# Performance work log

Hardware: AMD Instinct MI355X
Metric: run time of the kernel (lower is better)

The kernel has to match this reference:

```python
import jax, jax.numpy as jnp
import numpy as np

V, D, T, B, MS, WIN, EOS = 10000, 256, 128, 8, 4, 1, 4
S = MS + 1          # decoder segment length (y_input0 + MAX_SEGMENT tokens)
HRATE = 0.1
LOGINF = 1e6


def setup_inputs() -> dict:
    key = jax.random.key(0)
    ks = jax.random.split(key, 17)
    s = lambda i, shape: (jax.random.normal(ks[i], shape, jnp.float32) * 0.05)
    return dict(
        x_ids=jax.random.randint(ks[0], (B, T + 2 * WIN), 0, V),
        lens=jnp.full((B,), T, dtype=jnp.int32),
        emb=s(1, (V, D)),
        y_start=s(2, (1, D)),
        cell_Wi=s(3, (4 * D, D)), cell_Wh=s(4, (4 * D, D)), cell_b=s(5, (4 * D,)),
        yin0_W=s(6, (D, D)), yin0_b=s(7, (D,)),
        hlin_W=s(8, (2 * D, D)), hlin_b=s(9, (2 * D,)),
        l0_Wi=s(10, (4 * D, D)), l0_Wh=s(11, (4 * D, D)), l0_b=s(12, (4 * D,)),
        l1_Wi=s(13, (4 * D, D)), l1_Wh=s(14, (4 * D, D)), l1_b=s(15, (4 * D,)),
        out_b=s(16, (V,)),
    )


def _cell(x, h, c, Wi, Wh, b):
    # torch LSTM gate order: i, f, g, o
    g = x @ Wi.T + h @ Wh.T + b
    i, f, gg, o = jnp.split(g, 4, axis=-1)
    c2 = jax.nn.sigmoid(f) * c + jax.nn.sigmoid(i) * jnp.tanh(gg)
    return jax.nn.sigmoid(o) * jnp.tanh(c2), c2


def reference(x_ids, lens, emb, y_start, cell_Wi, cell_Wh, cell_b,
              yin0_W, yin0_b, hlin_W, hlin_b,
              l0_Wi, l0_Wh, l0_b, l1_Wi, l1_Wh, l1_b, out_b):
    y = x_ids[:, WIN:-WIN]                     # [B, T] target ids
    x = emb[y]                                 # [B, T, D]

    # --- encoder LSTMCell scan over j_start (state persists across schedule) ---
    seq = jnp.concatenate(
        [jnp.broadcast_to(y_start, (B, D))[None], jnp.transpose(x, (1, 0, 2))[:-1]], 0)  # [T,B,D]
    z = jnp.zeros((B, D), x.dtype)
    def enc_step(carry, xt):
        h, c = carry
        h2, c2 = _cell(xt, h, c, cell_Wi, cell_Wh, cell_b)
        return (h2, c2), h2
    _, h_seq = jax.lax.scan(enc_step, (z, z), seq)        # [T, B, D]

    drop_h = HRATE * h_seq
    y_in0 = drop_h @ yin0_W.T + yin0_b                    # [T, B, D]
    h0_all = jnp.tanh(drop_h @ hlin_W.T + hlin_b).reshape(T, B, 2, D)  # per-layer init h

    # --- build decoder inputs [T, B, S, D]: (y_input0, x[j_start:j_start+MS]) ---
    xp = jnp.pad(x, ((0, 0), (0, MS), (0, 0)))            # zero-pad time (causal => pads don't affect valid outputs)
    pos = jnp.arange(T)[:, None] + jnp.arange(MS)[None, :]           # [T, MS]
    seg_x = jnp.transpose(xp[:, pos], (1, 0, 2, 3))       # [T, B, MS, D]
    seg = jnp.concatenate([y_in0[:, :, None, :], seg_x], axis=2)     # [T, B, S, D]

    # --- 2-layer LSTM decoder, vmapped over j_start ---
    def decode(seg_t, h_init):                            # seg_t [B,S,D], h_init [B,2,D]
        def step(carry, xt):
            (h0, c0), (h1, c1) = carry
            h0n, c0n = _cell(xt, h0, c0, l0_Wi, l0_Wh, l0_b)
            h1n, c1n = _cell(h0n, h1, c1, l1_Wi, l1_Wh, l1_b)
            return ((h0n, c0n), (h1n, c1n)), h1n
        init = ((h_init[:, 0], z), (h_init[:, 1], z))
        _, hs = jax.lax.scan(step, init, jnp.transpose(seg_t, (1, 0, 2)))
        return jnp.transpose(hs, (1, 0, 2))               # [B, S, D]
    dec_h = jax.vmap(decode)(seg, h0_all)                 # [T, B, S, D]

    # --- tied output projection + log-softmax (only needed gathers kept) ---
    logits = jnp.einsum('tbsd,vd->tbsv', dec_h, emb) + out_b         # [T,B,S,V]
    logZ = jax.nn.logsumexp(logits, axis=-1)                          # [T,B,S]

    tgt = jnp.transpose(y[:, jnp.clip(pos, 0, T - 1)], (1, 0, 2))     # [T,B,MS]
    tgt_lp = jnp.take_along_axis(logits[:, :, :MS, :], tgt[..., None], axis=3)[..., 0] \
             - logZ[:, :, :MS]                                        # [T,B,MS]
    pmask = (pos < T)[:, None, :]
    cum = jnp.cumsum(jnp.where(pmask, tgt_lp, 0.0), axis=2)           # [T,B,MS]
    eos_lp = logits[:, :, 1:, EOS] - logZ[:, :, 1:]                   # [T,B,MS]

    kmask = (jnp.arange(T)[:, None] + jnp.arange(1, MS + 1)[None, :]) <= T   # [T,MS]
    body = jnp.where(kmask[:, None, :], cum + eos_lp, -LOGINF)        # [T,B,MS]
    logpy = jnp.concatenate([jnp.full((T, 1, B), -LOGINF, body.dtype),
                             jnp.transpose(body, (0, 2, 1))], axis=1)  # [T, MS+1, B]

    # --- alpha forward DP: alpha[j] = logsumexp_L alpha[j-L] + logpy[j-L][L] ---
    jj = jnp.arange(1, T + 1)[:, None]
    ii = jnp.arange(MS)[None, :]
    sstart = jj - MS + ii                                             # [T,MS]
    LPG = jnp.where((sstart >= 0)[..., None],
                    logpy[jnp.clip(sstart, 0), jnp.broadcast_to(MS - ii, (T, MS))],
                    -LOGINF)                                          # [T,MS,B]

    Apad0 = jnp.full((MS + T + 1, B), -LOGINF, logpy.dtype).at[MS].set(0.0)
    def dp_step(Apad, args):
        j, lpg = args
        win = jax.lax.dynamic_slice(Apad, (j, 0), (MS, B))            # alpha[j-MS .. j-1]
        aj = jax.nn.logsumexp(win + lpg, axis=0)
        return jax.lax.dynamic_update_slice(Apad, aj[None], (MS + j, 0)), None
    Apad, _ = jax.lax.scan(dp_step, Apad0, (jnp.arange(1, T + 1), LPG))
    alpha = Apad[MS:]                                                 # [T+1, B]

    ret = -jnp.sum(alpha[lens, jnp.arange(B)]) / jnp.sum(lens).astype(alpha.dtype)
    return ret
```

## Files before the change

### kernel.cpp

```cpp
#include <hip/hip_runtime.h>

#define V_ 10000
#define D_ 256
#define T_ 128
#define B_ 8
#define MS_ 4
#define S_ 5
#define EOS_ 4

typedef unsigned short b16_t;
typedef __attribute__((ext_vector_type(8))) short s16x8;
typedef __attribute__((ext_vector_type(8))) unsigned short u16x8;
typedef __attribute__((ext_vector_type(4))) float f32x4;
typedef __attribute__((ext_vector_type(2))) _Float16 h16x2;

__device__ inline b16_t f2bf(float f) {
  union { float f; unsigned u; } v; v.f = f;
  unsigned r = v.u + 0x7FFFu + ((v.u >> 16) & 1u);
  return (b16_t)(r >> 16);
}
__device__ inline float bf2f(b16_t h) {
  union { unsigned u; float f; } v; v.u = ((unsigned)h) << 16; return v.f;
}
__device__ inline float sigm_(float x) { return 1.0f / (1.0f + __expf(-x)); }
__device__ inline float tanh_(float x) { return 2.0f / (1.0f + __expf(-2.0f * x)) - 1.0f; }
__device__ inline h16x2 bch(unsigned u) { return __builtin_bit_cast(h16x2, u); }
__device__ inline unsigned pkh(float a, float b) {
  h16x2 v; v.x = (_Float16)a; v.y = (_Float16)b;
  return __builtin_bit_cast(unsigned, v);
}

#if __has_builtin(__builtin_amdgcn_fdot2)
#define FDOT2(a, b, c) __builtin_amdgcn_fdot2((a), (b), (c), false)
#else
#define FDOT2(a, b, c) ((c) + (float)(a).x * (float)(b).x + (float)(a).y * (float)(b).y)
#endif

__device__ inline void cvt4(const float* __restrict__ s, b16_t* __restrict__ d) {
  float4 v = *(const float4*)s;
  ushort4 o = { f2bf(v.x), f2bf(v.y), f2bf(v.z), f2bf(v.w) };
  *(ushort4*)d = o;
}

__global__ void k_prep(const float* __restrict__ emb, const float* __restrict__ cWi,
                       const float* __restrict__ y0W, const float* __restrict__ hlW,
                       const float* __restrict__ l0Wi, const float* __restrict__ l0Wh,
                       const float* __restrict__ l1Wi, const float* __restrict__ l1Wh,
                       const float* __restrict__ cWh, const int* __restrict__ x_ids,
                       const float* __restrict__ y_st,
                       b16_t* __restrict__ emb_bf, b16_t* __restrict__ cWi_bf,
                       b16_t* __restrict__ y0W_bf, b16_t* __restrict__ hlW_bf,
                       b16_t* __restrict__ l0Wi_bf, b16_t* __restrict__ l0Wh_bf,
                       b16_t* __restrict__ Wcat_bf, unsigned* __restrict__ Whf,
                       b16_t* __restrict__ x_bf, b16_t* __restrict__ seq_bf) {
  for (long i = (long)blockIdx.x * blockDim.x + threadIdx.x; i < 1213440L;
       i += (long)gridDim.x * blockDim.x) {
    if (i < 640000L) { cvt4(emb + i * 4, emb_bf + i * 4); }
    else if (i < 705536L) { long j = i - 640000L; cvt4(cWi + j * 4, cWi_bf + j * 4); }
    else if (i < 721920L) { long j = i - 705536L; cvt4(y0W + j * 4, y0W_bf + j * 4); }
    else if (i < 754688L) { long j = i - 721920L; cvt4(hlW + j * 4, hlW_bf + j * 4); }
    else if (i < 820224L) { long j = i - 754688L; cvt4(l0Wi + j * 4, l0Wi_bf + j * 4); }
    else if (i < 885760L) { long j = i - 820224L; cvt4(l0Wh + j * 4, l0Wh_bf + j * 4); }
    else if (i < 1016832L) {
      long j = (i - 885760L) * 4;
      long n = j >> 9; int k = (int)(j & 511);
      const float* src = (k < 256) ? (l1Wi + n * 256 + k) : (l1Wh + n * 256 + (k - 256));
      cvt4(src, Wcat_bf + j);
    } else if (i < 1082368L) {
      long j = i - 1016832L;
      float4 v = *(const float4*)(cWh + j * 4);
      Whf[2 * j] = pkh(v.x, v.y);
      Whf[2 * j + 1] = pkh(v.z, v.w);
    } else if (i < 1147904L) {
      long j = i - 1082368L;
      int bt = (int)(j >> 6), c = (int)(j & 63) * 4;
      int b = bt >> 7, t = bt & 127;
      int tok = x_ids[b * (T_ + 2) + t + 1];
      cvt4(emb + (size_t)tok * D_ + c, x_bf + (size_t)bt * D_ + c);
    } else {
      long j = i - 1147904L;
      int m = (int)(j >> 6), c = (int)(j & 63) * 4;
      int t = m >> 3, b = m & 7;
      const float* src = (t == 0) ? (y_st + c)
                                  : (emb + (size_t)x_ids[b * (T_ + 2) + t] * D_ + c);
      cvt4(src, seq_bf + (size_t)m * D_ + c);
    }
  }
}

__global__ __launch_bounds__(256) void k_gemm(const b16_t* __restrict__ A,
                                              const b16_t* __restrict__ Bw,
                                              const float* __restrict__ bias,
                                              float* __restrict__ C,
                                              int N, int act, int obf) {
  __shared__ b16_t As[64][264];
  __shared__ b16_t Bs[64][264];
  int tid = threadIdx.x;
  int rowBase = blockIdx.x * 64, colBase = blockIdx.y * 64;
  for (int i = tid; i < 64 * 32; i += 256) {
    int r = i >> 5, c = (i & 31) * 8;
    *(u16x8*)&As[r][c] = *(const u16x8*)(A + (size_t)(rowBase + r) * D_ + c);
    *(u16x8*)&Bs[r][c] = *(const u16x8*)(Bw + (size_t)(colBase + r) * D_ + c);
  }
  __syncthreads();
  int w = tid >> 6, l = tid & 63, lr = l & 15, kg = l >> 4;
  f32x4 acc[4] = {{0.f,0.f,0.f,0.f},{0.f,0.f,0.f,0.f},{0.f,0.f,0.f,0.f},{0.f,0.f,0.f,0.f}};
  for (int kk = 0; kk < 8; ++kk) {
    s16x8 a = *(const s16x8*)&As[w * 16 + lr][kk * 32 + kg * 8];
#pragma unroll
    for (int f = 0; f < 4; ++f) {
      s16x8 b = *(const s16x8*)&Bs[f * 16 + lr][kk * 32 + kg * 8];
      acc[f] = __builtin_amdgcn_mfma_f32_16x16x32_bf16(a, b, acc[f], 0, 0, 0);
    }
  }
#pragma unroll
  for (int f = 0; f < 4; ++f) {
#pragma unroll
    for (int r = 0; r < 4; ++r) {
      int m = rowBase + w * 16 + kg * 4 + r;
      int n = colBase + f * 16 + lr;
      float v = acc[f][r];
      if (bias) v += bias[n];
      if (act == 1) v = tanh_(v);
      size_t idx = (size_t)m * N + n;
      if (obf) ((b16_t*)C)[idx] = f2bf(v); else C[idx] = v;
    }
  }
}

__global__ __launch_bounds__(512, 2) void k_encoder(
    const unsigned* __restrict__ Whf,
    const float* __restrict__ encX,
    unsigned* __restrict__ hglob,
    int* __restrict__ flags,
    b16_t* __restrict__ droph) {
  int batch = blockIdx.x & 7, half = blockIdx.x >> 3;
  int tid = threadIdx.x;
  int gate = tid & 3, dl = tid >> 2;
  int dim = half * 128 + dl;
  int row = gate * 256 + dim;
  unsigned wv[128];
  {
    const uint4* wp = (const uint4*)(Whf + (size_t)row * 128);
#pragma unroll
    for (int i = 0; i < 32; ++i) {
      uint4 v = wp[i];
      wv[4 * i + 0] = v.x; wv[4 * i + 1] = v.y;
      wv[4 * i + 2] = v.z; wv[4 * i + 3] = v.w;
    }
  }
#pragma unroll
  for (int i = 0; i < 128; ++i) asm volatile("" : "+v"(wv[i]));

  __shared__ unsigned hbuf[2][128];
  if (tid < 256) ((unsigned*)hbuf)[tid] = 0;
  __syncthreads();

  float c = 0.f;
  int p = 0;
#pragma unroll 1
  for (int t = 0; t < 128; ++t) {
    float a = encX[((size_t)t * 8 + batch) * 1024 + row];
    uint4 hv[8];
#pragma unroll
    for (int i = 0; i < 8; ++i) hv[i] = *(const uint4*)&hbuf[p][i * 4];
    float s0 = 0.f, s1 = 0.f, s2 = 0.f, s3 = 0.f;
#pragma unroll
    for (int i = 0; i < 8; ++i) {
      s0 = FDOT2(bch(hv[i].x), bch(wv[4 * i + 0]), s0);
      s1 = FDOT2(bch(hv[i].y), bch(wv[4 * i + 1]), s1);
      s2 = FDOT2(bch(hv[i].z), bch(wv[4 * i + 2]), s2);
      s3 = FDOT2(bch(hv[i].w), bch(wv[4 * i + 3]), s3);
    }
    float acc = a + (s0 + s1) + (s2 + s3);
    int base = (tid & 63) & ~3;
    float gi = __shfl(acc, base + 0, 64);
    float gf = __shfl(acc, base + 1, 64);
    float gg = __shfl(acc, base + 2, 64);
    float go = __shfl(acc, base + 3, 64);
    float c2 = sigm_(gf) * c + sigm_(gi) * tanh_(gg);
    float h2 = sigm_(go) * tanh_(c2);
    c = c2;
    int q = p ^ 1;
    if (gate == 0) {
      ((_Float16*)hbuf[q])[dim] = (_Float16)h2;
      droph[((size_t)t * 8 + batch) * 256 + dim] = f2bf(0.1f * h2);
    }
    __syncthreads();
    if (t < 127) {
      if (tid < 64) {
        unsigned dw = hbuf[q][half * 64 + tid];
        __hip_atomic_store(&hglob[((size_t)(t + 1) * 8 + batch) * 128 + half * 64 + tid],
                           dw, __ATOMIC_RELAXED, __HIP_MEMORY_SCOPE_AGENT);
        asm volatile("s_waitcnt vmcnt(0)" ::: "memory");
        if (tid == 0)
          __hip_atomic_store(&flags[((t + 1) * 8 + batch) * 2 + half], 1,
                             __ATOMIC_RELAXED, __HIP_MEMORY_SCOPE_AGENT);
      } else if (tid < 128) {
        int lane = tid - 64;
        int* fp = &flags[((t + 1) * 8 + batch) * 2 + (1 - half)];
        while (__hip_atomic_load(fp, __ATOMIC_RELAXED, __HIP_MEMORY_SCOPE_AGENT) == 0)
          __builtin_amdgcn_s_sleep(1);
        asm volatile("" ::: "memory");
        unsigned dw = __hip_atomic_load(
            &hglob[((size_t)(t + 1) * 8 + batch) * 128 + (1 - half) * 64 + lane],
            __ATOMIC_RELAXED, __HIP_MEMORY_SCOPE_AGENT);
        hbuf[q][(1 - half) * 64 + lane] = dw;
      }
    }
    __syncthreads();
    p = q;
  }
}

__global__ void k_seg(const b16_t* __restrict__ x_bf, const b16_t* __restrict__ y_in0_bf,
                      b16_t* __restrict__ seg_bf) {
  int ps = blockIdx.x, d = threadIdx.x;
  int p = ps / S_, s = ps % S_;
  int t = p >> 3, b = p & 7;
  b16_t v;
  if (s == 0) v = y_in0_bf[(size_t)p * D_ + d];
  else {
    int tt = t + s - 1;
    v = (tt < T_) ? x_bf[((size_t)b * T_ + tt) * D_ + d] : (b16_t)0;
  }
  seg_bf[(size_t)ps * D_ + d] = v;
}

template <int K, int PHASE>
__global__ __launch_bounds__(512, 2) void k_dec_step(
    b16_t* __restrict__ hcat,
    const b16_t* __restrict__ Wbf,
    const float* __restrict__ X0,
    const float* __restrict__ bias,
    float* __restrict__ cst,
    b16_t* __restrict__ dec_out,
    int s) {
  __shared__ b16_t As[16][(K == 256) ? 264 : 520];
  __shared__ float gacc[16][1028];
  int tid = threadIdx.x;
  int R0 = blockIdx.x * 16;
  constexpr int CH = K / 8;
  for (int i = tid; i < 16 * CH; i += 512) {
    int r = i / CH, cc = (i % CH) * 8;
    *(u16x8*)&As[r][cc] = *(const u16x8*)(hcat + (size_t)(R0 + r) * 512 + cc);
  }
  __syncthreads();
  int w = tid >> 6, l = tid & 63, lr = l & 15, kg = l >> 4;
  int g = w >> 1, ch = w & 1;
  constexpr int NK = K / 32;
  s16x8 af[NK];
#pragma unroll
  for (int kk = 0; kk < NK; ++kk) af[kk] = *(const s16x8*)&As[lr][kk * 32 + kg * 8];
  int ncol0 = g * 256 + ch * 128;
  f32x4 acc[8];
#pragma unroll
  for (int nt = 0; nt < 8; ++nt) acc[nt] = f32x4{0.f, 0.f, 0.f, 0.f};
#pragma unroll
  for (int nt = 0; nt < 8; ++nt) {
    int n = ncol0 + nt * 16 + lr;
    const b16_t* bp = Wbf + (size_t)n * K + kg * 8;
#pragma unroll
    for (int kk = 0; kk < NK; ++kk) {
      s16x8 bf = *(const s16x8*)(bp + kk * 32);
      acc[nt] = __builtin_amdgcn_mfma_f32_16x16x32_bf16(af[kk], bf, acc[nt], 0, 0, 0);
    }
  }
#pragma unroll
  for (int nt = 0; nt < 8; ++nt)
#pragma unroll
    for (int r = 0; r < 4; ++r)
      gacc[kg * 4 + r][ncol0 + nt * 16 + lr] = acc[nt][r];
  __syncthreads();
  int rr = tid >> 5, dq = tid & 31;
  int pidx = R0 + rr;
#pragma unroll
  for (int u = 0; u < 8; ++u) {
    int d = u * 32 + dq;
    float gi = gacc[rr][d], gf = gacc[rr][256 + d];
    float gg = gacc[rr][512 + d], go = gacc[rr][768 + d];
    if (PHASE == 0) {
      const float* xp = X0 + ((size_t)pidx * 5 + s) * 1024;
      gi += xp[d]; gf += xp[256 + d]; gg += xp[512 + d]; go += xp[768 + d];
    } else {
      gi += bias[d]; gf += bias[256 + d]; gg += bias[512 + d]; go += bias[768 + d];
    }
    float c = cst[(size_t)pidx * 256 + d];
    float c2 = sigm_(gf) * c + sigm_(gi) * tanh_(gg);
    float h2 = sigm_(go) * tanh_(c2);
    cst[(size_t)pidx * 256 + d] = c2;
    b16_t hb = f2bf(h2);
    if (PHASE == 0) hcat[(size_t)pidx * 512 + d] = hb;
    else {
      hcat[(size_t)pidx * 512 + 256 + d] = hb;
      dec_out[((size_t)pidx * 5 + s) * 256 + d] = hb;
    }
  }
}

__global__ __launch_bounds__(512) void k_logits(const b16_t* __restrict__ Abf,
                                                const b16_t* __restrict__ emb_bf,
                                                const float* __restrict__ out_b,
                                                float* __restrict__ sumexp) {
  __shared__ b16_t Bs[64][264];
  int tid = threadIdx.x;
  int rowBase = blockIdx.x * 128;
  int w = tid >> 6, l = tid & 63, lr = l & 15, kg = l >> 4;
  s16x8 af[8];
  {
    const b16_t* arow = Abf + (size_t)(rowBase + w * 16 + lr) * 256;
#pragma unroll
    for (int kk = 0; kk < 8; ++kk) af[kk] = *(const s16x8*)(arow + kk * 32 + kg * 8);
  }
  float runsum[4] = {0.f, 0.f, 0.f, 0.f};
  int t0 = blockIdx.y * 23, t1 = (t0 + 23 < 157) ? (t0 + 23) : 157;
  for (int tile = t0; tile < t1; ++tile) {
    int colBase = tile * 64;
    __syncthreads();
    for (int i = tid; i < 64 * 32; i += 512) {
      int r = i >> 5, cc = (i & 31) * 8;
      int vrow = colBase + r;
      u16x8 bv = {0, 0, 0, 0, 0, 0, 0, 0};
      if (vrow < V_) bv = *(const u16x8*)(emb_bf + (size_t)vrow * D_ + cc);
      *(u16x8*)&Bs[r][cc] = bv;
    }
    __syncthreads();
    f32x4 acc[4] = {{0.f,0.f,0.f,0.f},{0.f,0.f,0.f,0.f},{0.f,0.f,0.f,0.f},{0.f,0.f,0.f,0.f}};
#pragma unroll
    for (int kk = 0; kk < 8; ++kk) {
#pragma unroll
      for (int f = 0; f < 4; ++f) {
        s16x8 b = *(const s16x8*)&Bs[f * 16 + lr][kk * 32 + kg * 8];
        acc[f] = __builtin_amdgcn_mfma_f32_16x16x32_bf16(af[kk], b, acc[f], 0, 0, 0);
      }
    }
#pragma unroll
    for (int f = 0; f < 4; ++f) {
      int n = colBase + f * 16 + lr;
      if (n < V_) {
        float ob = out_b[n];
#pragma unroll
        for (int r = 0; r < 4; ++r) runsum[r] += __expf(acc[f][r] + ob);
      }
    }
  }
#pragma unroll
  for (int r = 0; r < 4; ++r) {
    float rs = runsum[r];
    rs += __shfl_xor(rs, 1, 64);
    rs += __shfl_xor(rs, 2, 64);
    rs += __shfl_xor(rs, 4, 64);
    rs += __shfl_xor(rs, 8, 64);
    if (lr == 0) atomicAdd(&sumexp[rowBase + w * 16 + kg * 4 + r], rs);
  }
}

__global__ void k_extract(const b16_t* __restrict__ dec_h, const b16_t* __restrict__ emb_bf,
                          const float* __restrict__ out_b, const int* __restrict__ x_ids,
                          float* __restrict__ tl, float* __restrict__ el) {
  int p = blockIdx.x, lane = threadIdx.x;
  int t = p >> 3, b = p & 7;
  for (int s = 0; s < S_; ++s) {
    const b16_t* hr = dec_h + ((size_t)p * S_ + s) * D_;
    float hv[4];
#pragma unroll
    for (int j = 0; j < 4; ++j) hv[j] = bf2f(hr[lane * 4 + j]);
    if (s < MS_) {
      int pos = t + s; if (pos > T_ - 1) pos = T_ - 1;
      int tok = x_ids[b * (T_ + 2) + pos + 1];
      const b16_t* er = emb_bf + (size_t)tok * D_;
      float ps = 0.f;
#pragma unroll
      for (int j = 0; j < 4; ++j) ps += hv[j] * bf2f(er[lane * 4 + j]);
      for (int m = 1; m < 64; m <<= 1) ps += __shfl_xor(ps, m, 64);
      if (lane == 0) tl[p * MS_ + s] = ps + out_b[tok];
    }
    if (s >= 1) {
      const b16_t* er = emb_bf + (size_t)EOS_ * D_;
      float ps = 0.f;
#pragma unroll
      for (int j = 0; j < 4; ++j) ps += hv[j] * bf2f(er[lane * 4 + j]);
      for (int m = 1; m < 64; m <<= 1) ps += __shfl_xor(ps, m, 64);
      if (lane == 0) el[p * MS_ + (s - 1)] = ps + out_b[EOS_];
    }
  }
}

__global__ __launch_bounds__(256) void k_final(const float* __restrict__ sumexp,
                                               const float* __restrict__ tl,
                                               const float* __restrict__ el,
                                               const int* __restrict__ lens,
                                               float* __restrict__ out) {
  __shared__ float logpy[T_][S_][B_];
  __shared__ float alpha[T_ + 1][B_];
  int tid = threadIdx.x;
  for (int p = tid; p < T_ * B_; p += 256) {
    int t = p >> 3, b = p & 7;
    float lz[S_];
#pragma unroll
    for (int s = 0; s < S_; ++s) lz[s] = __logf(sumexp[p * S_ + s]);
    float cum = 0.f, cums[MS_];
#pragma unroll
    for (int s = 0; s < MS_; ++s) {
      float tlp = tl[p * MS_ + s] - lz[s];
      if (t + s < T_) cum += tlp;
      cums[s] = cum;
    }
#pragma unroll
    for (int k = 1; k <= MS_; ++k) {
      float bv = -1000000.0f;
      if (t + k <= T_) bv = cums[k - 1] + (el[p * MS_ + (k - 1)] - lz[k]);
      logpy[t][k][b] = bv;
    }
  }
  __syncthreads();
  if (tid < B_) {
    int b = tid;
    alpha[0][b] = 0.f;
    for (int j = 1; j <= T_; ++j) {
      float vs[MS_], vmax = -1e30f;
#pragma unroll
      for (int k = 1; k <= MS_; ++k) {
        float vv = -2000000.0f;
        if (j - k >= 0) vv = alpha[j - k][b] + logpy[j - k][k][b];
        vs[k - 1] = vv;
        if (vv > vmax) vmax = vv;
      }
      float ssum = 0.f;
#pragma unroll
      for (int k = 0; k < MS_; ++k) ssum += __expf(vs[k] - vmax);
      alpha[j][b] = vmax + __logf(ssum);
    }
  }
  __syncthreads();
  if (tid == 0) {
    float num = 0.f, den = 0.f;
    for (int b = 0; b < B_; ++b) { num += alpha[lens[b]][b]; den += (float)lens[b]; }
    out[0] = -num / den;
  }
}

extern "C" void kernel_launch(void* const* d_in, const int* in_sizes, int n_in,
                              void* d_out, int out_size, void* d_ws, size_t ws_size,
                              hipStream_t stream) {
  const int* x_ids   = (const int*)d_in[0];
  const int* lens    = (const int*)d_in[1];
  const float* emb   = (const float*)d_in[2];
  const float* y_st  = (const float*)d_in[3];
  const float* cWi   = (const float*)d_in[4];
  const float* cWh   = (const float*)d_in[5];
  const float* cb    = (const float*)d_in[6];
  const float* y0W   = (const float*)d_in[7];
  const float* y0b   = (const float*)d_in[8];
  const float* hlW   = (const float*)d_in[9];
  const float* hlb   = (const float*)d_in[10];
  const float* l0Wi  = (const float*)d_in[11];
  const float* l0Wh  = (const float*)d_in[12];
  const float* l0b   = (const float*)d_in[13];
  const float* l1Wi  = (const float*)d_in[14];
  const float* l1Wh  = (const float*)d_in[15];
  const float* l1b   = (const float*)d_in[16];
  const float* outb  = (const float*)d_in[17];
  float* out = (float*)d_out;
  (void)in_sizes; (void)n_in; (void)out_size; (void)ws_size;

  char* ws = (char*)d_ws;
  size_t cur = 0;
  auto alloc = [&](size_t bytes) { size_t o = cur; cur += (bytes + 255) & ~(size_t)255; return o; };
  b16_t* emb_bf    = (b16_t*)(ws + alloc((size_t)V_ * D_ * 2));
  b16_t* cWi_bf    = (b16_t*)(ws + alloc(1024 * 256 * 2));
  b16_t* y0W_bf    = (b16_t*)(ws + alloc(256 * 256 * 2));
  b16_t* hlW_bf    = (b16_t*)(ws + alloc(512 * 256 * 2));
  b16_t* l0Wi_bf   = (b16_t*)(ws + alloc(1024 * 256 * 2));
  b16_t* l0Wh_bf   = (b16_t*)(ws + alloc(1024 * 256 * 2));
  b16_t* Wcat_bf   = (b16_t*)(ws + alloc(1024 * 512 * 2));
  unsigned* Whf    = (unsigned*)(ws + alloc(1024 * 128 * 4));
  b16_t* x_bf      = (b16_t*)(ws + alloc((size_t)B_ * T_ * D_ * 2));
  b16_t* seq_bf    = (b16_t*)(ws + alloc(1024 * 256 * 2));
  float* encX      = (float*)(ws + alloc((size_t)1024 * 1024 * 4));
  b16_t* droph_bf  = (b16_t*)(ws + alloc(1024 * 256 * 2));
  b16_t* y_in0_bf  = (b16_t*)(ws + alloc(1024 * 256 * 2));
  b16_t* hcat      = (b16_t*)(ws + alloc(1024 * 512 * 2));
  b16_t* seg_bf    = (b16_t*)(ws + alloc((size_t)5120 * 256 * 2));
  float* X0        = (float*)(ws + alloc((size_t)5120 * 1024 * 4));
  float* c0        = (float*)(ws + alloc((size_t)2 * 1024 * 256 * 4));
  float* c1        = c0 + 1024 * 256;
  b16_t* dec_h_bf  = (b16_t*)(ws + alloc((size_t)5120 * 256 * 2));
  float* sumexp    = (float*)(ws + alloc(5120 * 4));
  int* flags       = (int*)(ws + alloc(129 * 8 * 2 * 4));
  unsigned* hglob  = (unsigned*)(ws + alloc((size_t)129 * 8 * 128 * 4));
  float* tl        = (float*)(ws + alloc(1024 * MS_ * 4));
  float* el        = (float*)(ws + alloc(1024 * MS_ * 4));

  hipMemsetAsync(sumexp, 0, 20480 + 8256, stream);
  hipMemsetAsync(c0, 0, (size_t)2 * 1024 * 256 * 4, stream);

  k_prep<<<1024, 256, 0, stream>>>(emb, cWi, y0W, hlW, l0Wi, l0Wh, l1Wi, l1Wh, cWh,
                                   x_ids, y_st,
                                   emb_bf, cWi_bf, y0W_bf, hlW_bf, l0Wi_bf, l0Wh_bf,
                                   Wcat_bf, Whf, x_bf, seq_bf);

  k_gemm<<<dim3(16, 16), 256, 0, stream>>>(seq_bf, cWi_bf, cb, encX, 1024, 0, 0);
  k_encoder<<<16, 512, 0, stream>>>(Whf, encX, hglob, flags, droph_bf);

  k_gemm<<<dim3(16, 4), 256, 0, stream>>>(droph_bf, y0W_bf, y0b, (float*)y_in0_bf, 256, 0, 1);
  k_gemm<<<dim3(16, 8), 256, 0, stream>>>(droph_bf, hlW_bf, hlb, (float*)hcat, 512, 1, 1);
  k_seg<<<5120, 256, 0, stream>>>(x_bf, y_in0_bf, seg_bf);
  k_gemm<<<dim3(80, 16), 256, 0, stream>>>(seg_bf, l0Wi_bf, l0b, X0, 1024, 0, 0);

  for (int s = 0; s < S_; ++s) {
    k_dec_step<256, 0><<<64, 512, 0, stream>>>(hcat, l0Wh_bf, X0, nullptr, c0, nullptr, s);
    k_dec_step<512, 1><<<64, 512, 0, stream>>>(hcat, Wcat_bf, nullptr, l1b, c1, dec_h_bf, s);
  }

  k_logits<<<dim3(40, 7), 512, 0, stream>>>(dec_h_bf, emb_bf, outb, sumexp);
  k_extract<<<1024, 64, 0, stream>>>(dec_h_bf, emb_bf, outb, x_ids, tl, el);
  k_final<<<1, 256, 0, stream>>>(sumexp, tl, el, lens, out);
}
```

Before: 676.8 us.

## Single-block encoder per batch, overlap X0 GEMM with encoder, fuse decoder layers

The encoder now uses one 512-thread block per batch row, holding the recurrent weights in registers plus LDS instead of splitting across two blocks that synchronise through global flags. Extra blocks in the same launch compute the token-dependent part of the layer-0 input projection while the serial encoder runs. The y_in0 column of that projection is done later with strided GEMM calls. Segment building moves into the prep kernel, the two decoder layers are fused into one kernel per step, and the logits grid is split finer. This removes inter-block spin-waits and several launches, at the cost of higher register and LDS pressure and fewer blocks in the decoder.

```diff
diff --git a/kernel.cpp b/kernel.cpp
--- a/kernel.cpp
+++ b/kernel.cpp
@@ -52,8 +52,8 @@
                        b16_t* __restrict__ y0W_bf, b16_t* __restrict__ hlW_bf,
                        b16_t* __restrict__ l0Wi_bf, b16_t* __restrict__ l0Wh_bf,
                        b16_t* __restrict__ Wcat_bf, unsigned* __restrict__ Whf,
-                       b16_t* __restrict__ x_bf, b16_t* __restrict__ seq_bf) {
-  for (long i = (long)blockIdx.x * blockDim.x + threadIdx.x; i < 1213440L;
+                       b16_t* __restrict__ seq_bf, b16_t* __restrict__ seg_bf) {
+  for (long i = (long)blockIdx.x * blockDim.x + threadIdx.x; i < 1410048L;
        i += (long)gridDim.x * blockDim.x) {
     if (i < 640000L) { cvt4(emb + i * 4, emb_bf + i * 4); }
     else if (i < 705536L) { long j = i - 640000L; cvt4(cWi + j * 4, cWi_bf + j * 4); }
@@ -73,34 +73,42 @@
       Whf[2 * j + 1] = pkh(v.z, v.w);
     } else if (i < 1147904L) {
       long j = i - 1082368L;
-      int bt = (int)(j >> 6), c = (int)(j & 63) * 4;
-      int b = bt >> 7, t = bt & 127;
-      int tok = x_ids[b * (T_ + 2) + t + 1];
-      cvt4(emb + (size_t)tok * D_ + c, x_bf + (size_t)bt * D_ + c);
-    } else {
-      long j = i - 1147904L;
       int m = (int)(j >> 6), c = (int)(j & 63) * 4;
       int t = m >> 3, b = m & 7;
       const float* src = (t == 0) ? (y_st + c)
                                   : (emb + (size_t)x_ids[b * (T_ + 2) + t] * D_ + c);
       cvt4(src, seq_bf + (size_t)m * D_ + c);
-    }
-  }
-}
-
-__global__ __launch_bounds__(256) void k_gemm(const b16_t* __restrict__ A,
+    } else {
+      long j = i - 1147904L;
+      int r = (int)(j >> 6), c = (int)(j & 63) * 4;
+      int p = r >> 2, s = 1 + (r & 3);
+      int t = p >> 3, b = p & 7;
+      int tt = t + s - 1;
+      int ps = r + (r >> 2) + 1;
+      if (tt < T_) {
+        int tok = x_ids[b * (T_ + 2) + tt + 1];
+        cvt4(emb + (size_t)tok * D_ + c, seg_bf + (size_t)ps * 256 + c);
+      } else {
+        ushort4 z = {0, 0, 0, 0};
+        *(ushort4*)(seg_bf + (size_t)ps * 256 + c) = z;
+      }
+    }
+  }
+}
+
+__global__ __launch_bounds__(256) void k_gemm(const b16_t* __restrict__ A, int lda,
                                               const b16_t* __restrict__ Bw,
                                               const float* __restrict__ bias,
-                                              float* __restrict__ C,
-                                              int N, int act, int obf) {
+                                              float* __restrict__ C, int ldc,
+                                              int act, int obf) {
   __shared__ b16_t As[64][264];
   __shared__ b16_t Bs[64][264];
   int tid = threadIdx.x;
   int rowBase = blockIdx.x * 64, colBase = blockIdx.y * 64;
   for (int i = tid; i < 64 * 32; i += 256) {
     int r = i >> 5, c = (i & 31) * 8;
-    *(u16x8*)&As[r][c] = *(const u16x8*)(A + (size_t)(rowBase + r) * D_ + c);
-    *(u16x8*)&Bs[r][c] = *(const u16x8*)(Bw + (size_t)(colBase + r) * D_ + c);
+    *(u16x8*)&As[r][c] = *(const u16x8*)(A + (size_t)(rowBase + r) * lda + c);
+    *(u16x8*)&Bs[r][c] = *(const u16x8*)(Bw + (size_t)(colBase + r) * 256 + c);
   }
   __syncthreads();
   int w = tid >> 6, l = tid & 63, lr = l & 15, kg = l >> 4;
@@ -122,178 +130,224 @@
       float v = acc[f][r];
       if (bias) v += bias[n];
       if (act == 1) v = tanh_(v);
-      size_t idx = (size_t)m * N + n;
+      size_t idx = (size_t)m * ldc + n;
       if (obf) ((b16_t*)C)[idx] = f2bf(v); else C[idx] = v;
     }
   }
 }
 
-__global__ __launch_bounds__(512, 2) void k_encoder(
-    const unsigned* __restrict__ Whf,
-    const float* __restrict__ encX,
-    unsigned* __restrict__ hglob,
-    int* __restrict__ flags,
-    b16_t* __restrict__ droph) {
-  int batch = blockIdx.x & 7, half = blockIdx.x >> 3;
+struct EncSmem { uint4 wtail4[16][512]; unsigned hbuf[128]; float gl[1024]; };
+struct GemSmem { b16_t As[64][264]; };
+
+__global__ __launch_bounds__(512, 2) void k_enc_x0(
+    const unsigned* __restrict__ Whf, const float* __restrict__ encX,
+    b16_t* __restrict__ droph,
+    const b16_t* __restrict__ seg_bf, const b16_t* __restrict__ l0Wi_bf,
+    const float* __restrict__ l0b, float* __restrict__ X0) {
+  __shared__ union { EncSmem e; GemSmem g; } sm;
   int tid = threadIdx.x;
-  int gate = tid & 3, dl = tid >> 2;
-  int dim = half * 128 + dl;
-  int row = gate * 256 + dim;
-  unsigned wv[128];
-  {
-    const uint4* wp = (const uint4*)(Whf + (size_t)row * 128);
-#pragma unroll
-    for (int i = 0; i < 32; ++i) {
-      uint4 v = wp[i];
-      wv[4 * i + 0] = v.x; wv[4 * i + 1] = v.y;
-      wv[4 * i + 2] = v.z; wv[4 * i + 3] = v.w;
-    }
-  }
-#pragma unroll
-  for (int i = 0; i < 128; ++i) asm volatile("" : "+v"(wv[i]));
-
-  __shared__ unsigned hbuf[2][128];
-  if (tid < 256) ((unsigned*)hbuf)[tid] = 0;
-  __syncthreads();
-
-  float c = 0.f;
-  int p = 0;
+  if (blockIdx.x < 8) {
+    int batch = blockIdx.x;
+    int r0 = tid, r1 = tid + 512;
+    unsigned wa[96], wb[96];
+    {
+      const uint4* p0 = (const uint4*)(Whf + (size_t)r0 * 128);
+      const uint4* p1 = (const uint4*)(Whf + (size_t)r1 * 128);
+#pragma unroll
+      for (int i = 0; i < 24; ++i) {
+        uint4 v = p0[i];
+        wa[4*i] = v.x; wa[4*i+1] = v.y; wa[4*i+2] = v.z; wa[4*i+3] = v.w;
+      }
+#pragma unroll
+      for (int i = 0; i < 24; ++i) {
+        uint4 v = p1[i];
+        wb[4*i] = v.x; wb[4*i+1] = v.y; wb[4*i+2] = v.z; wb[4*i+3] = v.w;
+      }
+#pragma unroll
+      for (int i = 0; i < 8; ++i) sm.e.wtail4[i][tid] = p0[24 + i];
+#pragma unroll
+      for (int i = 0; i < 8; ++i) sm.e.wtail4[8 + i][tid] = p1[24 + i];
+    }
+#pragma unroll
+    for (int i = 0; i < 96; ++i) asm volatile("v_mov_b32 %0, %0" : "+v"(wa[i]));
+#pragma unroll
+    for (int i = 0; i < 96; ++i) asm volatile("v_mov_b32 %0, %0" : "+v"(wb[i]));
+    if (tid < 128) sm.e.hbuf[tid] = 0;
+    float c = 0.f;
+    __syncthreads();
 #pragma unroll 1
-  for (int t = 0; t < 128; ++t) {
-    float a = encX[((size_t)t * 8 + batch) * 1024 + row];
-    uint4 hv[8];
-#pragma unroll
-    for (int i = 0; i < 8; ++i) hv[i] = *(const uint4*)&hbuf[p][i * 4];
-    float s0 = 0.f, s1 = 0.f, s2 = 0.f, s3 = 0.f;
-#pragma unroll
-    for (int i = 0; i < 8; ++i) {
-      s0 = FDOT2(bch(hv[i].x), bch(wv[4 * i + 0]), s0);
-      s1 = FDOT2(bch(hv[i].y), bch(wv[4 * i + 1]), s1);
-      s2 = FDOT2(bch(hv[i].z), bch(wv[4 * i + 2]), s2);
-      s3 = FDOT2(bch(hv[i].w), bch(wv[4 * i + 3]), s3);
-    }
-    float acc = a + (s0 + s1) + (s2 + s3);
-    int base = (tid & 63) & ~3;
-    float gi = __shfl(acc, base + 0, 64);
-    float gf = __shfl(acc, base + 1, 64);
-    float gg = __shfl(acc, base + 2, 64);
-    float go = __shfl(acc, base + 3, 64);
-    float c2 = sigm_(gf) * c + sigm_(gi) * tanh_(gg);
-    float h2 = sigm_(go) * tanh_(c2);
-    c = c2;
-    int q = p ^ 1;
-    if (gate == 0) {
-      ((_Float16*)hbuf[q])[dim] = (_Float16)h2;
-      droph[((size_t)t * 8 + batch) * 256 + dim] = f2bf(0.1f * h2);
+    for (int t = 0; t < 128; ++t) {
+      const float* ex = encX + ((size_t)t * 8 + batch) * 1024;
+      float a0 = ex[r0], a1 = ex[r1];
+      float s0 = 0.f, s1 = 0.f, s2 = 0.f, s3 = 0.f;
+#pragma unroll
+      for (int j = 0; j < 24; ++j) {
+        uint4 hv = *(const uint4*)&sm.e.hbuf[4 * j];
+        s0 = FDOT2(bch(hv.x), bch(wa[4*j+0]), s0);
+        s0 = FDOT2(bch(hv.y), bch(wa[4*j+1]), s0);
+        s1 = FDOT2(bch(hv.z), bch(wa[4*j+2]), s1);
+        s1 = FDOT2(bch(hv.w), bch(wa[4*j+3]), s1);
+        s2 = FDOT2(bch(hv.x), bch(wb[4*j+0]), s2);
+        s2 = FDOT2(bch(hv.y), bch(wb[4*j+1]), s2);
+        s3 = FDOT2(bch(hv.z), bch(wb[4*j+2]), s3);
+        s3 = FDOT2(bch(hv.w), bch(wb[4*j+3]), s3);
+      }
+#pragma unroll
+      for (int j = 0; j < 8; ++j) {
+        uint4 hv = *(const uint4*)&sm.e.hbuf[96 + 4 * j];
+        uint4 w0 = sm.e.wtail4[j][tid];
+        uint4 w1 = sm.e.wtail4[8 + j][tid];
+        s0 = FDOT2(bch(hv.x), bch(w0.x), s0);
+        s0 = FDOT2(bch(hv.y), bch(w0.y), s0);
+        s1 = FDOT2(bch(hv.z), bch(w0.z), s1);
+        s1 = FDOT2(bch(hv.w), bch(w0.w), s1);
+        s2 = FDOT2(bch(hv.x), bch(w1.x), s2);
+        s2 = FDOT2(bch(hv.y), bch(w1.y), s2);
+        s3 = FDOT2(bch(hv.z), bch(w1.z), s3);
+        s3 = FDOT2(bch(hv.w), bch(w1.w), s3);
+      }
+      sm.e.gl[r0] = a0 + s0 + s1;
+      sm.e.gl[r1] = a1 + s2 + s3;
+      __syncthreads();
+      if (tid < 256) {
+        float gi = sm.e.gl[tid],       gf = sm.e.gl[256 + tid];
+        float gg = sm.e.gl[512 + tid], go = sm.e.gl[768 + tid];
+        float c2 = sigm_(gf) * c + sigm_(gi) * tanh_(gg);
+        float h2 = sigm_(go) * tanh_(c2);
+        c = c2;
+        droph[((size_t)t * 8 + batch) * 256 + tid] = f2bf(0.1f * h2);
+        ((_Float16*)sm.e.hbuf)[tid] = (_Float16)h2;
+      }
+      __syncthreads();
+    }
+  } else {
+    int g = blockIdx.x - 8;
+    int j0 = g * 64;
+    for (int i = tid; i < 64 * 32; i += 512) {
+      int r = i >> 5, cc = (i & 31) * 8;
+      int jj = j0 + r, ps = jj + (jj >> 2) + 1;
+      *(u16x8*)&sm.g.As[r][cc] = *(const u16x8*)(seg_bf + (size_t)ps * 256 + cc);
     }
     __syncthreads();
-    if (t < 127) {
-      if (tid < 64) {
-        unsigned dw = hbuf[q][half * 64 + tid];
-        __hip_atomic_store(&hglob[((size_t)(t + 1) * 8 + batch) * 128 + half * 64 + tid],
-                           dw, __ATOMIC_RELAXED, __HIP_MEMORY_SCOPE_AGENT);
-        asm volatile("s_waitcnt vmcnt(0)" ::: "memory");
-        if (tid == 0)
-          __hip_atomic_store(&flags[((t + 1) * 8 + batch) * 2 + half], 1,
-                             __ATOMIC_RELAXED, __HIP_MEMORY_SCOPE_AGENT);
-      } else if (tid < 128) {
-        int lane = tid - 64;
-        int* fp = &flags[((t + 1) * 8 + batch) * 2 + (1 - half)];
-        while (__hip_atomic_load(fp, __ATOMIC_RELAXED, __HIP_MEMORY_SCOPE_AGENT) == 0)
-          __builtin_amdgcn_s_sleep(1);
-        asm volatile("" ::: "memory");
-        unsigned dw = __hip_atomic_load(
-            &hglob[((size_t)(t + 1) * 8 + batch) * 128 + (1 - half) * 64 + lane],
-            __ATOMIC_RELAXED, __HIP_MEMORY_SCOPE_AGENT);
-        hbuf[q][(1 - half) * 64 + lane] = dw;
-      }
-    }
-    __syncthreads();
-    p = q;
-  }
-}
-
-__global__ void k_seg(const b16_t* __restrict__ x_bf, const b16_t* __restrict__ y_in0_bf,
-                      b16_t* __restrict__ seg_bf) {
-  int ps = blockIdx.x, d = threadIdx.x;
-  int p = ps / S_, s = ps % S_;
-  int t = p >> 3, b = p & 7;
-  b16_t v;
-  if (s == 0) v = y_in0_bf[(size_t)p * D_ + d];
-  else {
-    int tt = t + s - 1;
-    v = (tt < T_) ? x_bf[((size_t)b * T_ + tt) * D_ + d] : (b16_t)0;
-  }
-  seg_bf[(size_t)ps * D_ + d] = v;
-}
-
-template <int K, int PHASE>
-__global__ __launch_bounds__(512, 2) void k_dec_step(
+    int w = tid >> 6, l = tid & 63, lr = l & 15, kg = l >> 4;
+    int mt = w & 3, hn = w >> 2;
+    s16x8 af[8];
+#pragma unroll
+    for (int kk = 0; kk < 8; ++kk)
+      af[kk] = *(const s16x8*)&sm.g.As[mt * 16 + lr][kk * 32 + kg * 8];
+#pragma unroll 1
+    for (int nb = 0; nb < 4; ++nb) {
+      int nc0 = hn * 512 + nb * 128;
+      f32x4 acc[8];
+#pragma unroll
+      for (int nt = 0; nt < 8; ++nt) acc[nt] = f32x4{0.f, 0.f, 0.f, 0.f};
+#pragma unroll
+      for (int nt = 0; nt < 8; ++nt) {
+        int n = nc0 + nt * 16 + lr;
+        const b16_t* bp = l0Wi_bf + (size_t)n * 256 + kg * 8;
+#pragma unroll
+        for (int kk = 0; kk < 8; ++kk)
+          acc[nt] = __builtin_amdgcn_mfma_f32_16x16x32_bf16(
+              af[kk], *(const s16x8*)(bp + kk * 32), acc[nt], 0, 0, 0);
+      }
+#pragma unroll
+      for (int nt = 0; nt < 8; ++nt) {
+        int n = nc0 + nt * 16 + lr;
+        float ob = l0b[n];
+#pragma unroll
+        for (int r = 0; r < 4; ++r) {
+          int jj = j0 + mt * 16 + kg * 4 + r;
+          int ps = jj + (jj >> 2) + 1;
+          X0[(size_t)ps * 1024 + n] = acc[nt][r] + ob;
+        }
+      }
+    }
+  }
+}
+
+__global__ __launch_bounds__(512) void k_dec2(
     b16_t* __restrict__ hcat,
-    const b16_t* __restrict__ Wbf,
+    const b16_t* __restrict__ l0Wh_bf,
+    const b16_t* __restrict__ Wcat_bf,
     const float* __restrict__ X0,
-    const float* __restrict__ bias,
-    float* __restrict__ cst,
-    b16_t* __restrict__ dec_out,
-    int s) {
-  __shared__ b16_t As[16][(K == 256) ? 264 : 520];
-  __shared__ float gacc[16][1028];
+    const float* __restrict__ l1b,
+    float* __restrict__ c0, float* __restrict__ c1,
+    b16_t* __restrict__ dec_out, int s) {
+  __shared__ b16_t A0s[32][264];
+  __shared__ b16_t A1s[32][520];
   int tid = threadIdx.x;
-  int R0 = blockIdx.x * 16;
-  constexpr int CH = K / 8;
-  for (int i = tid; i < 16 * CH; i += 512) {
-    int r = i / CH, cc = (i % CH) * 8;
-    *(u16x8*)&As[r][cc] = *(const u16x8*)(hcat + (size_t)(R0 + r) * 512 + cc);
+  int R0 = blockIdx.x * 32;
+  for (int i = tid; i < 32 * 32; i += 512) {
+    int r = i >> 5, cc = (i & 31) * 8;
+    *(u16x8*)&A0s[r][cc] = *(const u16x8*)(hcat + (size_t)(R0 + r) * 512 + cc);
+    *(u16x8*)&A1s[r][256 + cc] = *(const u16x8*)(hcat + (size_t)(R0 + r) * 512 + 256 + cc);
   }
   __syncthreads();
   int w = tid >> 6, l = tid & 63, lr = l & 15, kg = l >> 4;
-  int g = w >> 1, ch = w & 1;
-  constexpr int NK = K / 32;
-  s16x8 af[NK];
-#pragma unroll
-  for (int kk = 0; kk < NK; ++kk) af[kk] = *(const s16x8*)&As[lr][kk * 32 + kg * 8];
-  int ncol0 = g * 256 + ch * 128;
-  f32x4 acc[8];
-#pragma unroll
-  for (int nt = 0; nt < 8; ++nt) acc[nt] = f32x4{0.f, 0.f, 0.f, 0.f};
-#pragma unroll
-  for (int nt = 0; nt < 8; ++nt) {
-    int n = ncol0 + nt * 16 + lr;
-    const b16_t* bp = Wbf + (size_t)n * K + kg * 8;
-#pragma unroll
-    for (int kk = 0; kk < NK; ++kk) {
-      s16x8 bf = *(const s16x8*)(bp + kk * 32);
-      acc[nt] = __builtin_amdgcn_mfma_f32_16x16x32_bf16(af[kk], bf, acc[nt], 0, 0, 0);
-    }
-  }
-#pragma unroll
-  for (int nt = 0; nt < 8; ++nt)
-#pragma unroll
-    for (int r = 0; r < 4; ++r)
-      gacc[kg * 4 + r][ncol0 + nt * 16 + lr] = acc[nt][r];
+  int m2 = w & 1, dg = w >> 1;
+  s16x8 af[8];
+#pragma unroll
+  for (int kk = 0; kk < 8; ++kk)
+    af[kk] = *(const s16x8*)&A0s[m2 * 16 + lr][kk * 32 + kg * 8];
+#pragma unroll 1
+  for (int dt = 0; dt < 4; ++dt) {
+    int d = dg * 64 + dt * 16 + lr;
+    f32x4 ai{}, afv{}, ag{}, ao{};
+#pragma unroll
+    for (int kk = 0; kk < 8; ++kk) {
+      ai  = __builtin_amdgcn_mfma_f32_16x16x32_bf16(af[kk],
+              *(const s16x8*)(l0Wh_bf + (size_t)(d) * 256 + kk * 32 + kg * 8), ai, 0, 0, 0);
+      afv = __builtin_amdgcn_mfma_f32_16x16x32_bf16(af[kk],
+              *(const s16x8*)(l0Wh_bf + (size_t)(256 + d) * 256 + kk * 32 + kg * 8), afv, 0, 0, 0);
+      ag  = __builtin_amdgcn_mfma_f32_16x16x32_bf16(af[kk],
+              *(const s16x8*)(l0Wh_bf + (size_t)(512 + d) * 256 + kk * 32 + kg * 8), ag, 0, 0, 0);
+      ao  = __builtin_amdgcn_mfma_f32_16x16x32_bf16(af[kk],
+              *(const s16x8*)(l0Wh_bf + (size_t)(768 + d) * 256 + kk * 32 + kg * 8), ao, 0, 0, 0);
+    }
+#pragma unroll
+    for (int r = 0; r < 4; ++r) {
+      int p = R0 + m2 * 16 + kg * 4 + r;
+      const float* xp = X0 + ((size_t)p * 5 + s) * 1024;
+      float gi = ai[r] + xp[d],        gf = afv[r] + xp[256 + d];
+      float gg = ag[r] + xp[512 + d],  go = ao[r] + xp[768 + d];
+      float c = c0[(size_t)p * 256 + d];
+      float c2 = sigm_(gf) * c + sigm_(gi) * tanh_(gg);
+      float h2 = sigm_(go) * tanh_(c2);
+      c0[(size_t)p * 256 + d] = c2;
+      b16_t hb = f2bf(h2);
+      A1s[m2 * 16 + kg * 4 + r][d] = hb;
+      hcat[(size_t)p * 512 + d] = hb;
+    }
+  }
   __syncthreads();
-  int rr = tid >> 5, dq = tid & 31;
-  int pidx = R0 + rr;
-#pragma unroll
-  for (int u = 0; u < 8; ++u) {
-    int d = u * 32 + dq;
-    float gi = gacc[rr][d], gf = gacc[rr][256 + d];
-    float gg = gacc[rr][512 + d], go = gacc[rr][768 + d];
-    if (PHASE == 0) {
-      const float* xp = X0 + ((size_t)pidx * 5 + s) * 1024;
-      gi += xp[d]; gf += xp[256 + d]; gg += xp[512 + d]; go += xp[768 + d];
-    } else {
-      gi += bias[d]; gf += bias[256 + d]; gg += bias[512 + d]; go += bias[768 + d];
-    }
-    float c = cst[(size_t)pidx * 256 + d];
-    float c2 = sigm_(gf) * c + sigm_(gi) * tanh_(gg);
-    float h2 = sigm_(go) * tanh_(c2);
-    cst[(size_t)pidx * 256 + d] = c2;
-    b16_t hb = f2bf(h2);
-    if (PHASE == 0) hcat[(size_t)pidx * 512 + d] = hb;
-    else {
-      hcat[(size_t)pidx * 512 + 256 + d] = hb;
-      dec_out[((size_t)pidx * 5 + s) * 256 + d] = hb;
+#pragma unroll 1
+  for (int dt = 0; dt < 4; ++dt) {
+    int d = dg * 64 + dt * 16 + lr;
+    f32x4 ai{}, afv{}, ag{}, ao{};
+#pragma unroll
+    for (int kk = 0; kk < 16; ++kk) {
+      s16x8 a2 = *(const s16x8*)&A1s[m2 * 16 + lr][kk * 32 + kg * 8];
+      ai  = __builtin_amdgcn_mfma_f32_16x16x32_bf16(a2,
+              *(const s16x8*)(Wcat_bf + (size_t)(d) * 512 + kk * 32 + kg * 8), ai, 0, 0, 0);
+      afv = __builtin_amdgcn_mfma_f32_16x16x32_bf16(a2,
+              *(const s16x8*)(Wcat_bf + (size_t)(256 + d) * 512 + kk * 32 + kg * 8), afv, 0, 0, 0);
+      ag  = __builtin_amdgcn_mfma_f32_16x16x32_bf16(a2,
+              *(const s16x8*)(Wcat_bf + (size_t)(512 + d) * 512 + kk * 32 + kg * 8), ag, 0, 0, 0);
+      ao  = __builtin_amdgcn_mfma_f32_16x16x32_bf16(a2,
+              *(const s16x8*)(Wcat_bf + (size_t)(768 + d) * 512 + kk * 32 + kg * 8), ao, 0, 0, 0);
+    }
+#pragma unroll
+    for (int r = 0; r < 4; ++r) {
+      int p = R0 + m2 * 16 + kg * 4 + r;
+      float gi = ai[r] + l1b[d],        gf = afv[r] + l1b[256 + d];
+      float gg = ag[r] + l1b[512 + d],  go = ao[r] + l1b[768 + d];
+      float c = c1[(size_t)p * 256 + d];
+      float c2 = sigm_(gf) * c + sigm_(gi) * tanh_(gg);
+      float h2 = sigm_(go) * tanh_(c2);
+      c1[(size_t)p * 256 + d] = c2;
+      b16_t hb = f2bf(h2);
+      hcat[(size_t)p * 512 + 256 + d] = hb;
+      dec_out[((size_t)p * 5 + s) * 256 + d] = hb;
     }
   }
 }
@@ -313,7 +367,7 @@
     for (int kk = 0; kk < 8; ++kk) af[kk] = *(const s16x8*)(arow + kk * 32 + kg * 8);
   }
   float runsum[4] = {0.f, 0.f, 0.f, 0.f};
-  int t0 = blockIdx.y * 23, t1 = (t0 + 23 < 157) ? (t0 + 23) : 157;
+  int t0 = blockIdx.y * 12, t1 = (t0 + 12 < 157) ? (t0 + 12) : 157;
   for (int tile = t0; tile < t1; ++tile) {
     int colBase = tile * 64;
     __syncthreads();
@@ -475,11 +529,9 @@
   b16_t* l0Wh_bf   = (b16_t*)(ws + alloc(1024 * 256 * 2));
   b16_t* Wcat_bf   = (b16_t*)(ws + alloc(1024 * 512 * 2));
   unsigned* Whf    = (unsigned*)(ws + alloc(1024 * 128 * 4));
-  b16_t* x_bf      = (b16_t*)(ws + alloc((size_t)B_ * T_ * D_ * 2));
   b16_t* seq_bf    = (b16_t*)(ws + alloc(1024 * 256 * 2));
   float* encX      = (float*)(ws + alloc((size_t)1024 * 1024 * 4));
   b16_t* droph_bf  = (b16_t*)(ws + alloc(1024 * 256 * 2));
-  b16_t* y_in0_bf  = (b16_t*)(ws + alloc(1024 * 256 * 2));
   b16_t* hcat      = (b16_t*)(ws + alloc(1024 * 512 * 2));
   b16_t* seg_bf    = (b16_t*)(ws + alloc((size_t)5120 * 256 * 2));
   float* X0        = (float*)(ws + alloc((size_t)5120 * 1024 * 4));
@@ -487,33 +539,30 @@
   float* c1        = c0 + 1024 * 256;
   b16_t* dec_h_bf  = (b16_t*)(ws + alloc((size_t)5120 * 256 * 2));
   float* sumexp    = (float*)(ws + alloc(5120 * 4));
-  int* flags       = (int*)(ws + alloc(129 * 8 * 2 * 4));
-  unsigned* hglob  = (unsigned*)(ws + alloc((size_t)129 * 8 * 128 * 4));
   float* tl        = (float*)(ws + alloc(1024 * MS_ * 4));
   float* el        = (float*)(ws + alloc(1024 * MS_ * 4));
 
-  hipMemsetAsync(sumexp, 0, 20480 + 8256, stream);
+  hipMemsetAsync(sumexp, 0, 5120 * 4, stream);
   hipMemsetAsync(c0, 0, (size_t)2 * 1024 * 256 * 4, stream);
 
   k_prep<<<1024, 256, 0, stream>>>(emb, cWi, y0W, hlW, l0Wi, l0Wh, l1Wi, l1Wh, cWh,
                                    x_ids, y_st,
                                    emb_bf, cWi_bf, y0W_bf, hlW_bf, l0Wi_bf, l0Wh_bf,
-                                   Wcat_bf, Whf, x_bf, seq_bf);
-
-  k_gemm<<<dim3(16, 16), 256, 0, stream>>>(seq_bf, cWi_bf, cb, encX, 1024, 0, 0);
-  k_encoder<<<16, 512, 0, stream>>>(Whf, encX, hglob, flags, droph_bf);
-
-  k_gemm<<<dim3(16, 4), 256, 0, stream>>>(droph_bf, y0W_bf, y0b, (float*)y_in0_bf, 256, 0, 1);
-  k_gemm<<<dim3(16, 8), 256, 0, stream>>>(droph_bf, hlW_bf, hlb, (float*)hcat, 512, 1, 1);
-  k_seg<<<5120, 256, 0, stream>>>(x_bf, y_in0_bf, seg_bf);
-  k_gemm<<<dim3(80, 16), 256, 0, stream>>>(seg_bf, l0Wi_bf, l0b, X0, 1024, 0, 0);
-
-  for (int s = 0; s < S_; ++s) {
-    k_dec_step<256, 0><<<64, 512, 0, stream>>>(hcat, l0Wh_bf, X0, nullptr, c0, nullptr, s);
-    k_dec_step<512, 1><<<64, 512, 0, stream>>>(hcat, Wcat_bf, nullptr, l1b, c1, dec_h_bf, s);
-  }
-
-  k_logits<<<dim3(40, 7), 512, 0, stream>>>(dec_h_bf, emb_bf, outb, sumexp);
+                                   Wcat_bf, Whf, seq_bf, seg_bf);
+
+  k_gemm<<<dim3(16, 16), 256, 0, stream>>>(seq_bf, 256, cWi_bf, cb, encX, 1024, 0, 0);
+  k_enc_x0<<<72, 512, 0, stream>>>(Whf, encX, droph_bf, seg_bf, l0Wi_bf, l0b, X0);
+
+  k_gemm<<<dim3(16, 4), 256, 0, stream>>>(droph_bf, 256, y0W_bf, y0b,
+                                          (float*)seg_bf, 1280, 0, 1);
+  k_gemm<<<dim3(16, 8), 256, 0, stream>>>(droph_bf, 256, hlW_bf, hlb,
+                                          (float*)hcat, 512, 1, 1);
+  k_gemm<<<dim3(16, 16), 256, 0, stream>>>(seg_bf, 1280, l0Wi_bf, l0b, X0, 5120, 0, 0);
+
+  for (int s = 0; s < S_; ++s)
+    k_dec2<<<32, 512, 0, stream>>>(hcat, l0Wh_bf, Wcat_bf, X0, l1b, c0, c1, dec_h_bf, s);
+
+  k_logits<<<dim3(40, 14), 512, 0, stream>>>(dec_h_bf, emb_bf, outb, sumexp);
   k_extract<<<1024, 64, 0, stream>>>(dec_h_bf, emb_bf, outb, x_ids, tl, el);
   k_final<<<1, 256, 0, stream>>>(sumexp, tl, el, lens, out);
 }
```

Measured after the change: 897.8 us. +32.7%, slower.
